# Optimization experiments

Hardware: AMD Instinct MI355X
Metric: run time of the kernel (lower is better)

The kernel has to match this reference:

```python
import jax, jax.numpy as jnp
import numpy as np

N = 30000      # nodes
E = 480000     # edges
H = 128        # hidden_nf
NQ = 7         # qubits
D = 2 ** NQ    # 128, quantum state dim == embedding_size
NL = 2         # block n_layers (QGCL layers)
QL = 2         # quantum circuit layers inside each QGCL
NORM = 100.0   # normalization_factor ('sum' aggregation)
NORM_CONST = 1.0


def _cnot_perm_indices(n):
    # Composed permutation for CNOT(0,1)...CNOT(n-2,n-1), CNOT(n-1,0).
    # PennyLane convention: wire 0 is the most significant bit.
    idx = np.arange(2 ** n)
    pairs = [(i, i + 1) for i in range(n - 1)] + [(n - 1, 0)]
    g = None
    for c, t in pairs:
        cb = (idx >> (n - 1 - c)) & 1
        f = idx ^ (cb << (n - 1 - t))  # flip target bit if control set (involution)
        g = f if g is None else g[f]
    return g

_CNOT_G = jnp.asarray(_cnot_perm_indices(NQ))


def _quantum_states(q_in, coeffs, A_re, A_im):
    """Vectorized VQC over all nodes. q_in [N,D] real -> [N,D] complex state."""
    norm = jnp.sqrt(jnp.sum(q_in ** 2, axis=1, keepdims=True) + 1e-12)
    s = (q_in / norm).astype(jnp.complex64)  # normalized initial state per node
    I = jnp.eye(D, dtype=jnp.complex64)
    for j in range(QL):
        # Cayley transform -> unitary
        A = (A_re[j] + 1j * A_im[j]).astype(jnp.complex64)
        A = A + A.conj().T
        q = (A - 1j * I) @ jnp.linalg.inv(A + 1j * I)
        # single-qubit layer: RY(b) @ RX(a) on every qubit -> kron power
        a, b = coeffs[j, 0].astype(jnp.complex64), coeffs[j, 1].astype(jnp.complex64)
        ca, sa = jnp.cos(a / 2), jnp.sin(a / 2)
        cb, sb = jnp.cos(b / 2), jnp.sin(b / 2)
        RX = jnp.stack([jnp.stack([ca, -1j * sa]), jnp.stack([-1j * sa, ca])])
        RY = jnp.stack([jnp.stack([cb, -sb]), jnp.stack([sb, cb])])
        G = RY @ RX
        Gk = G
        for _ in range(NQ - 1):
            Gk = jnp.kron(Gk, G)
        s = s @ q.T            # QubitUnitary
        s = s @ Gk.T           # RX/RY on all qubits
        s = s[:, _CNOT_G]      # CNOT ring (pure permutation)
    return s


def setup_inputs() -> dict:
    key = jax.random.key(0)
    ks = jax.random.split(key, 20)
    return {
        "h": jax.random.normal(ks[0], (N, H), jnp.float32),
        "x": jax.random.normal(ks[1], (N, 3), jnp.float32),
        "edge_index": jax.random.randint(ks[2], (2, E), 0, N, jnp.int32),
        "edge_attr": jax.random.normal(ks[3], (E, 1), jnp.float32),
        "e_w1": jax.random.normal(ks[4], (NL, 2 * H + 2, H), jnp.float32) * 0.05,
        "e_b1": jnp.zeros((NL, H), jnp.float32),
        "e_w2": jax.random.normal(ks[5], (NL, H, H), jnp.float32) * 0.05,
        "e_b2": jnp.zeros((NL, H), jnp.float32),
        "enc_w": jax.random.normal(ks[6], (NL, 2 * H, D), jnp.float32) * 0.05,
        "enc_b": jnp.zeros((NL, D), jnp.float32),
        "coeffs": jax.random.normal(ks[7], (NL, QL, 2), jnp.float32) * 0.1,
        "A_re": jax.random.normal(ks[8], (NL, QL, D, D), jnp.float32) * 0.01,
        "A_im": jax.random.normal(ks[9], (NL, QL, D, D), jnp.float32) * 0.01,
        "dec_w": jax.random.normal(ks[10], (NL, D, H), jnp.float32) * 0.05,
        "dec_b": jnp.zeros((NL, H), jnp.float32),
        "c_w1": jax.random.normal(ks[11], (2 * H + 2, H), jnp.float32) * 0.05,
        "c_b1": jnp.zeros((H,), jnp.float32),
        "c_w2": jax.random.normal(ks[12], (H, H), jnp.float32) * 0.05,
        "c_b2": jnp.zeros((H,), jnp.float32),
        "c_w3": jax.random.normal(ks[13], (H, 1), jnp.float32) * 0.001,  # xavier gain=0.001
    }


def reference(h, x, edge_index, edge_attr, e_w1, e_b1, e_w2, e_b2, enc_w, enc_b,
              coeffs, A_re, A_im, dec_w, dec_b, c_w1, c_b1, c_w2, c_b2, c_w3):
    row, col = edge_index[0], edge_index[1]
    # coord2diff
    diff = x[row] - x[col]
    radial = jnp.sum(diff ** 2, axis=1, keepdims=True)     # [E,1] (used as 'distances')
    coord_diff = diff / (jnp.sqrt(radial + 1e-8) + NORM_CONST)
    eattr = jnp.concatenate([radial, edge_attr], axis=1)   # [E,2]

    for l in range(NL):  # QGCL layers
        m = jnp.concatenate([h[row], h[col], eattr], axis=1)       # [E, 2H+2]
        m = jax.nn.silu(m @ e_w1[l] + e_b1[l])
        m = jax.nn.silu(m @ e_w2[l] + e_b2[l])                     # edge messages mij
        agg = jax.ops.segment_sum(m, row, num_segments=N) / NORM   # scatter-add
        q_in = jnp.concatenate([h, agg], axis=1) @ enc_w[l] + enc_b[l]
        # quantum part is detached in the original (torch .detach + re-tensor)
        qs = jax.lax.stop_gradient(
            _quantum_states(q_in, coeffs[l], A_re[l], A_im[l]))
        h = h + qs.real.astype(h.dtype) @ dec_w[l] + dec_b[l]

    # EquivariantUpdate (tanh=False)
    t = jnp.concatenate([h[row], h[col], eattr], axis=1)
    t = jax.nn.silu(t @ c_w1 + c_b1)
    t = jax.nn.silu(t @ c_w2 + c_b2)
    t = t @ c_w3                                                   # [E,1]
    trans = coord_diff * t
    x = x + jax.ops.segment_sum(trans, row, num_segments=N) / NORM
    return h, x
```

## Files before the change

### kernel.cpp

```cpp
#include <hip/hip_runtime.h>
#include <math.h>

#define N_NODES 30000
#define N_EDGES 480000
#define HDIM 128
#define EPB 64
#define AS 296
#define NAS 264
#define MS 136

typedef __attribute__((ext_vector_type(8))) short short8b;
typedef __attribute__((ext_vector_type(4))) float f32x4;

__device__ __forceinline__ float silu_f(float v) {
  return v / (1.0f + __expf(-v));
}

__device__ __forceinline__ unsigned short f2bf(float f) {
  unsigned int u = __float_as_uint(f);
  unsigned int r = u + 0x7fffu + ((u >> 16) & 1u);
  return (unsigned short)(r >> 16);
}

__global__ void init_out_kernel(const float* __restrict__ h,
                                const float* __restrict__ x,
                                float* __restrict__ out) {
  int idx = blockIdx.x * 256 + threadIdx.x;
  out[idx] = h[idx];
  if (idx < N_NODES * 3) out[N_NODES * HDIM + idx] = x[idx];
}

__global__ void h_to_bf_kernel(const float* __restrict__ h,
                               ushort* __restrict__ hbf) {
  int idx = blockIdx.x * 256 + threadIdx.x;
  float4 v = ((const float4*)h)[idx];
  ushort4 o;
  o.x = f2bf(v.x); o.y = f2bf(v.y); o.z = f2bf(v.z); o.w = f2bf(v.w);
  ((ushort4*)hbf)[idx] = o;
}

__global__ void convert_w_kernel(const float* __restrict__ W,
                                 ushort* __restrict__ dst, int Kreal, int KT) {
  int idx = blockIdx.x * 256 + threadIdx.x;
  if (idx >= KT * 4096) return;
  int kt = idx >> 12, rem = idx & 4095, n = rem >> 5, kk = rem & 31;
  int k = kt * 32 + kk;
  float v = (k < Kreal) ? W[(size_t)k * HDIM + n] : 0.0f;
  dst[idx] = f2bf(v);
}

__global__ void count_kernel(const int* __restrict__ ei, int* __restrict__ cursor) {
  int e = blockIdx.x * 256 + threadIdx.x;
  atomicAdd(&cursor[ei[e]], 1);
}

__global__ __launch_bounds__(1024) void scan_kernel(int* __restrict__ cursor,
                                                    int* __restrict__ cstart) {
  __shared__ int sums[1024];
  const int tid = threadIdx.x;
  const int base = tid * 30;
  int local[30];
  int s = 0;
#pragma unroll
  for (int j = 0; j < 30; ++j) {
    int idx = base + j;
    int d = (idx < N_NODES) ? cursor[idx] : 0;
    local[j] = s;
    s += d;
  }
  sums[tid] = s;
  __syncthreads();
  for (int off = 1; off < 1024; off <<= 1) {
    int add = (tid >= off) ? sums[tid - off] : 0;
    __syncthreads();
    sums[tid] += add;
    __syncthreads();
  }
  int excl = (tid == 0) ? 0 : sums[tid - 1];
#pragma unroll
  for (int j = 0; j < 30; ++j) {
    int idx = base + j;
    if (idx < N_NODES) {
      int v = excl + local[j];
      cursor[idx] = v;
      cstart[idx] = v;
    }
  }
}

__global__ void fill_kernel(const int* __restrict__ ei, int* __restrict__ cursor,
                            int* __restrict__ elist) {
// ... 115 lines not shown
  gkm[(size_t)lj * 16384 + idx] = acc;
}

__global__ void nj_kernel(const float2* __restrict__ qm,
                          const float2* __restrict__ gkm,
                          const int* __restrict__ g,
                          float2* __restrict__ njm) {
  int lj = blockIdx.y;
  int idx = blockIdx.x * 256 + threadIdx.x;
  int i = idx >> 7, c = idx & 127;
  int gc = g[c];
  const float2* q = qm + (size_t)lj * 16384;
  const float2* gk = gkm + (size_t)lj * 16384;
  float2 acc = make_float2(0.f, 0.f);
  for (int k = 0; k < 128; ++k) {
    float2 qa = q[k * 128 + i];
    float2 gb = gk[gc * 128 + k];
    acc.x += qa.x * gb.x - qa.y * gb.y;
    acc.y += qa.x * gb.y + qa.y * gb.x;
  }
  njm[(size_t)lj * 16384 + idx] = acc;
}

__global__ void compose_kernel(const float2* __restrict__ njm,
                               float2* __restrict__ um) {
  int l = blockIdx.y;
  int idx = blockIdx.x * 256 + threadIdx.x;
  int i = idx >> 7, c = idx & 127;
  const float2* n0 = njm + (size_t)(l * 2 + 0) * 16384;
  const float2* n1 = njm + (size_t)(l * 2 + 1) * 16384;
  float2 acc = make_float2(0.f, 0.f);
  for (int k = 0; k < 128; ++k) {
    float2 a = n0[i * 128 + k];
    float2 b = n1[k * 128 + c];
    acc.x += a.x * b.x - a.y * b.y;
    acc.y += a.x * b.y + a.y * b.x;
  }
  um[(size_t)l * 16384 + idx] = acc;
}

__global__ void wqd_kernel(const float2* __restrict__ um,
                           const float* __restrict__ decw,
                           float* __restrict__ wqd) {
  int l = blockIdx.y;
  int idx = blockIdx.x * 256 + threadIdx.x;
  int i = idx >> 7, c = idx & 127;
  const float2* u = um + (size_t)l * 16384;
  const float* dw = decw + (size_t)l * 16384;
  float acc = 0.f;
  for (int k = 0; k < 128; ++k) acc += u[i * 128 + k].x * dw[k * 128 + c];
  wqd[(size_t)l * 16384 + idx] = acc;
}

__global__ __launch_bounds__(256, 4) void edge_mfma_kernel(
    const ushort* __restrict__ hbf, const int* __restrict__ ei,
    const float* __restrict__ x, const float* __restrict__ ea,
    const int* __restrict__ elist, const int* __restrict__ cstart,
    const ushort* __restrict__ w1cs, const float* __restrict__ b1,
    const ushort* __restrict__ w2cs, const float* __restrict__ b2,
    float* __restrict__ agg, float* __restrict__ headp) {
  __shared__ ushort A[EPB * AS];
  __shared__ int rows[EPB];
  ushort* m1 = A;
  float* m2 = (float*)A;

  const int tid = threadIdx.x;
  const int lane = tid & 63, wave = tid >> 6;
  const int lrow = lane & 15, lq = lane >> 4;
  const int wbase = wave * 32;
  const int woff0 = (wbase + lrow) * 32 + lq * 8;
  const int woff1 = (wbase + 16 + lrow) * 32 + lq * 8;

  const float b1v[2] = {b1[wbase + lrow], b1[wbase + 16 + lrow]};
  const float b2v[2] = {b2[wbase + lrow], b2[wbase + 16 + lrow]};

  const int i0 = blockIdx.x * EPB;
  {
    const int e = tid >> 2, j = tid & 3;
    const int edge = elist[i0 + e];
    const int r = ei[edge], c = ei[N_EDGES + edge];
    if (j == 0) rows[e] = r;
    const uint4* hr = (const uint4*)(hbf + (size_t)r * HDIM + j * 32);
    const uint4* hc = (const uint4*)(hbf + (size_t)c * HDIM + j * 32);
    uint4* d1 = (uint4*)(A + e * AS + j * 32);
    uint4* d2 = (uint4*)(A + e * AS + 128 + j * 32);
    d1[0] = hr[0]; d1[1] = hr[1]; d1[2] = hr[2]; d1[3] = hr[3];
    d2[0] = hc[0]; d2[1] = hc[1]; d2[2] = hc[2]; d2[3] = hc[3];
    if (j == 3) {
      float dx = x[r * 3 + 0] - x[c * 3 + 0];
      float dy = x[r * 3 + 1] - x[c * 3 + 1];
      float dz = x[r * 3 + 2] - x[c * 3 + 2];
      ushort* dst = A + e * AS;
      dst[256] = f2bf(dx * dx + dy * dy + dz * dz);
      dst[257] = f2bf(ea[edge]);
#pragma unroll
      for (int z = 258; z < 288; ++z) dst[z] = 0;
    }
  }
  __syncthreads();

  f32x4 acc[4][2];
#pragma unroll
  for (int mt = 0; mt < 4; ++mt)
#pragma unroll
    for (int nt = 0; nt < 2; ++nt) acc[mt][nt] = (f32x4){0.f, 0.f, 0.f, 0.f};
  {
    short8b wcur0 = *(const short8b*)(w1cs + woff0);
    short8b wcur1 = *(const short8b*)(w1cs + woff1);
#pragma unroll
    for (int kt = 0; kt < 9; ++kt) {
      short8b wn0, wn1;
      if (kt < 8) {
        wn0 = *(const short8b*)(w1cs + (kt + 1) * 4096 + woff0);
        wn1 = *(const short8b*)(w1cs + (kt + 1) * 4096 + woff1);
      }
      short8b af[4];
#pragma unroll
      for (int mt = 0; mt < 4; ++mt)
        af[mt] = *(const short8b*)(A + (mt * 16 + lrow) * AS + kt * 32 + lq * 8);
#pragma unroll
      for (int mt = 0; mt < 4; ++mt) {
        acc[mt][0] = __builtin_amdgcn_mfma_f32_16x16x32_bf16(af[mt], wcur0, acc[mt][0], 0, 0, 0);
        acc[mt][1] = __builtin_amdgcn_mfma_f32_16x16x32_bf16(af[mt], wcur1, acc[mt][1], 0, 0, 0);
      }
      if (kt < 8) { wcur0 = wn0; wcur1 = wn1; }
    }
  }
  __syncthreads();
#pragma unroll
  for (int mt = 0; mt < 4; ++mt)
#pragma unroll
    for (int nt = 0; nt < 2; ++nt)
#pragma unroll
      for (int r = 0; r < 4; ++r)
        m1[(mt * 16 + lq * 4 + r) * MS + wbase + nt * 16 + lrow] =
            f2bf(silu_f(acc[mt][nt][r] + b1v[nt]));
  __syncthreads();

  f32x4 acc2[4][2];
#pragma unroll
  for (int mt = 0; mt < 4; ++mt)
#pragma unroll
    for (int nt = 0; nt < 2; ++nt) acc2[mt][nt] = (f32x4){0.f, 0.f, 0.f, 0.f};
  {
    short8b wcur0 = *(const short8b*)(w2cs + woff0);
    short8b wcur1 = *(const short8b*)(w2cs + woff1);
#pragma unroll
    for (int kt = 0; kt < 4; ++kt) {
      short8b wn0, wn1;
      if (kt < 3) {
        wn0 = *(const short8b*)(w2cs + (kt + 1) * 4096 + woff0);
        wn1 = *(const short8b*)(w2cs + (kt + 1) * 4096 + woff1);
      }
      short8b af[4];
#pragma unroll
      for (int mt = 0; mt < 4; ++mt)
        af[mt] = *(const short8b*)(m1 + (mt * 16 + lrow) * MS + kt * 32 + lq * 8);
#pragma unroll
      for (int mt = 0; mt < 4; ++mt) {
        acc2[mt][0] = __builtin_amdgcn_mfma_f32_16x16x32_bf16(af[mt], wcur0, acc2[mt][0], 0, 0, 0);
        acc2[mt][1] = __builtin_amdgcn_mfma_f32_16x16x32_bf16(af[mt], wcur1, acc2[mt][1], 0, 0, 0);
      }
      if (kt < 3) { wcur0 = wn0; wcur1 = wn1; }
    }
  }
  __syncthreads();
#pragma unroll
  for (int mt = 0; mt < 4; ++mt)
#pragma unroll
    for (int nt = 0; nt < 2; ++nt)
#pragma unroll
      for (int r = 0; r < 4; ++r)
        m2[(mt * 16 + lq * 4 + r) * MS + wbase + nt * 16 + lrow] =
            silu_f(acc2[mt][nt][r] + b2v[nt]);
  __syncthreads();

  const int e2 = tid & 63, cg = tid >> 6, cb = cg * 32;
  const int r_e = rows[e2];
  const bool leader = (e2 == 0) || (rows[e2 - 1] != r_e);
  if (leader) {
    f32x4 sum[8];
#pragma unroll
    for (int q = 0; q < 8; ++q) sum[q] = *(const f32x4*)(m2 + e2 * MS + cb + q * 4);
    int f = e2 + 1;
    while (f < EPB && rows[f] == r_e) {
#pragma unroll
      for (int q = 0; q < 8; ++q) sum[q] += *(const f32x4*)(m2 + f * MS + cb + q * 4);
      ++f;
    }
    float* dst = (e2 == 0 && cstart[r_e] < i0)
                     ? headp + (size_t)blockIdx.x * HDIM + cb
                     : agg + (size_t)r_e * HDIM + cb;
#pragma unroll
    for (int q = 0; q < 8; ++q) *(f32x4*)(dst + q * 4) = sum[q];
  }
}

__global__ __launch_bounds__(256, 2) void node_mfma_kernel(
    float* __restrict__ out_h, const float* __restrict__ agg,
    const int* __restrict__ cstart, const int* __restrict__ cend,
    const float* __restrict__ headp,
    const ushort* __restrict__ enccs, const float* __restrict__ encb,
    const ushort* __restrict__ wqdcs, const float* __restrict__ decb,
    ushort* __restrict__ hbf) {
  __shared__ ushort A[EPB * NAS];
  __shared__ ushort m1[EPB * MS];
  __shared__ float nbuf[4 * EPB];
  const int tid = threadIdx.x;
  const int n0 = blockIdx.x * EPB;

  const int lane = tid & 63, wave = tid >> 6;
  const int lrow = lane & 15, lq = lane >> 4;
  const int wbase = wave * 32;

  short8b wef[8][2], wqf[4][2];
#pragma unroll
  for (int kt = 0; kt < 8; ++kt)
#pragma unroll
    for (int nt = 0; nt < 2; ++nt)
      wef[kt][nt] = *(const short8b*)(enccs + kt * 4096 + (wbase + nt * 16 + lrow) * 32 + lq * 8);
#pragma unroll
  for (int kt = 0; kt < 4; ++kt)
#pragma unroll
    for (int nt = 0; nt < 2; ++nt)
      wqf[kt][nt] = *(const short8b*)(wqdcs + kt * 4096 + (wbase + nt * 16 + lrow) * 32 + lq * 8);
  const float ebv[2] = {encb[wbase + lrow], encb[wbase + 16 + lrow]};
  const float dbv[2] = {decb[wbase + lrow], decb[wbase + 16 + lrow]};

  {
    const int e = tid >> 2, j = tid & 3;
    int node = n0 + e;
    if (node >= N_NODES) node = N_NODES - 1;
    if (j < 2) {
      const float4* s4 = (const float4*)(out_h + (size_t)node * HDIM + j * 64);
      ushort* dst = A + e * NAS + j * 64;
#pragma unroll
      for (int i = 0; i < 16; ++i) {
        float4 v = s4[i];
        ushort4 o;
        o.x = f2bf(v.x); o.y = f2bf(v.y); o.z = f2bf(v.z); o.w = f2bf(v.w);
        ((ushort4*)dst)[i] = o;
      }
    } else {
      const int s = cstart[node], en = cend[node];
      const bool hasAgg = en > s;
      const float4* a4 = (const float4*)(agg + (size_t)node * HDIM + (j - 2) * 64);
      const int bb0 = (s >> 6) + 1;
      const int bb1 = hasAgg ? ((en - 1) >> 6) : 0;
      ushort* dst = A + e * NAS + 128 + (j - 2) * 64;
#pragma unroll
      for (int i = 0; i < 16; ++i) {
        float4 v = hasAgg ? a4[i] : make_float4(0.f, 0.f, 0.f, 0.f);
        for (int bb = bb0; bb <= bb1; ++bb) {
          float4 hv = *(const float4*)(headp + (size_t)bb * HDIM + (j - 2) * 64 + i * 4);
          v.x += hv.x; v.y += hv.y; v.z += hv.z; v.w += hv.w;
        }
        ushort4 o;
        o.x = f2bf(v.x * 0.01f); o.y = f2bf(v.y * 0.01f);
        o.z = f2bf(v.z * 0.01f); o.w = f2bf(v.w * 0.01f);
        ((ushort4*)dst)[i] = o;
      }
    }
  }
  __syncthreads();

  f32x4 acc[4][2];
#pragma unroll
  for (int mt = 0; mt < 4; ++mt)
#pragma unroll
    for (int nt = 0; nt < 2; ++nt) acc[mt][nt] = (f32x4){0.f, 0.f, 0.f, 0.f};
#pragma unroll
  for (int kt = 0; kt < 8; ++kt) {
    short8b af[4];
#pragma unroll
    for (int mt = 0; mt < 4; ++mt)
      af[mt] = *(const short8b*)(A + (mt * 16 + lrow) * NAS + kt * 32 + lq * 8);
#pragma unroll
    for (int mt = 0; mt < 4; ++mt)
#pragma unroll
      for (int nt = 0; nt < 2; ++nt)
        acc[mt][nt] = __builtin_amdgcn_mfma_f32_16x16x32_bf16(af[mt], wef[kt][nt], acc[mt][nt], 0, 0, 0);
  }
#pragma unroll
  for (int mt = 0; mt < 4; ++mt) {
    float ssp[4] = {0.f, 0.f, 0.f, 0.f};
#pragma unroll
    for (int nt = 0; nt < 2; ++nt)
#pragma unroll
      for (int r = 0; r < 4; ++r) {
        acc[mt][nt][r] += ebv[nt];
        ssp[r] += acc[mt][nt][r] * acc[mt][nt][r];
      }
#pragma unroll
    for (int m = 1; m < 16; m <<= 1)
#pragma unroll
      for (int r = 0; r < 4; ++r) ssp[r] += __shfl_xor(ssp[r], m, 64);
    if (lrow == 0) {
#pragma unroll
      for (int r = 0; r < 4; ++r)
        nbuf[wave * EPB + mt * 16 + lq * 4 + r] = ssp[r];
    }
  }
  __syncthreads();
#pragma unroll
  for (int mt = 0; mt < 4; ++mt)
#pragma unroll
    for (int r = 0; r < 4; ++r) {
      const int row = mt * 16 + lq * 4 + r;
      float sum = nbuf[row] + nbuf[EPB + row] + nbuf[2 * EPB + row] + nbuf[3 * EPB + row];
      float inv = 1.0f / sqrtf(sum + 1e-12f);
#pragma unroll
      for (int nt = 0; nt < 2; ++nt)
        m1[row * MS + wbase + nt * 16 + lrow] = f2bf(acc[mt][nt][r] * inv);
    }
  __syncthreads();

  f32x4 acc2[4][2];
#pragma unroll
  for (int mt = 0; mt < 4; ++mt)
#pragma unroll
    for (int nt = 0; nt < 2; ++nt) acc2[mt][nt] = (f32x4){0.f, 0.f, 0.f, 0.f};
#pragma unroll
  for (int kt = 0; kt < 4; ++kt) {
    short8b af[4];
#pragma unroll
    for (int mt = 0; mt < 4; ++mt)
      af[mt] = *(const short8b*)(m1 + (mt * 16 + lrow) * MS + kt * 32 + lq * 8);
#pragma unroll
    for (int mt = 0; mt < 4; ++mt)
#pragma unroll
      for (int nt = 0; nt < 2; ++nt)
        acc2[mt][nt] = __builtin_amdgcn_mfma_f32_16x16x32_bf16(af[mt], wqf[kt][nt], acc2[mt][nt], 0, 0, 0);
  }
#pragma unroll
  for (int mt = 0; mt < 4; ++mt)
#pragma unroll
    for (int nt = 0; nt < 2; ++nt) {
      const int n = wbase + nt * 16 + lrow;
#pragma unroll
      for (int r = 0; r < 4; ++r) {
        const int node = n0 + mt * 16 + lq * 4 + r;
        if (node < N_NODES) {
          size_t off = (size_t)node * HDIM + n;
          float hn = out_h[off] + acc2[mt][nt][r] + dbv[nt];
          out_h[off] = hn;
          hbf[off] = f2bf(hn);
        }
      }
    }
}

__global__ __launch_bounds__(256, 4) void coord_mfma_kernel(
    const ushort* __restrict__ hbf, const int* __restrict__ ei,
    const float* __restrict__ x, const float* __restrict__ ea,
    const int* __restrict__ elist,
    const ushort* __restrict__ w1cs, const float* __restrict__ b1,
    const ushort* __restrict__ w2cs, const float* __restrict__ b2,
    const float* __restrict__ w3, float* __restrict__ xout) {
  __shared__ ushort A[EPB * AS];
  __shared__ int rows[EPB];
  __shared__ int colsA[EPB];
  __shared__ float pbuf[4 * EPB];
  __shared__ float tv[EPB];
  ushort* m1 = A;

  const int tid = threadIdx.x;
  const int lane = tid & 63, wave = tid >> 6;
  const int lrow = lane & 15, lq = lane >> 4;
  const int wbase = wave * 32;
  const int woff0 = (wbase + lrow) * 32 + lq * 8;
  const int woff1 = (wbase + 16 + lrow) * 32 + lq * 8;

  const float b1v[2] = {b1[wbase + lrow], b1[wbase + 16 + lrow]};
  const float b2v[2] = {b2[wbase + lrow], b2[wbase + 16 + lrow]};
  const float w3v[2] = {w3[wbase + lrow], w3[wbase + 16 + lrow]};

  const int i0 = blockIdx.x * EPB;
  {
    const int e = tid >> 2, j = tid & 3;
    const int edge = elist[i0 + e];
    const int r = ei[edge], c = ei[N_EDGES + edge];
    if (j == 0) { rows[e] = r; colsA[e] = c; }
    const uint4* hr = (const uint4*)(hbf + (size_t)r * HDIM + j * 32);
    const uint4* hc = (const uint4*)(hbf + (size_t)c * HDIM + j * 32);
    uint4* d1 = (uint4*)(A + e * AS + j * 32);
    uint4* d2 = (uint4*)(A + e * AS + 128 + j * 32);
    d1[0] = hr[0]; d1[1] = hr[1]; d1[2] = hr[2]; d1[3] = hr[3];
    d2[0] = hc[0]; d2[1] = hc[1]; d2[2] = hc[2]; d2[3] = hc[3];
    if (j == 3) {
      float dx = x[r * 3 + 0] - x[c * 3 + 0];
      float dy = x[r * 3 + 1] - x[c * 3 + 1];
      float dz = x[r * 3 + 2] - x[c * 3 + 2];
      ushort* dst = A + e * AS;
      dst[256] = f2bf(dx * dx + dy * dy + dz * dz);
      dst[257] = f2bf(ea[edge]);
#pragma unroll
      for (int z = 258; z < 288; ++z) dst[z] = 0;
    }
  }
  __syncthreads();

  f32x4 acc[4][2];
#pragma unroll
  for (int mt = 0; mt < 4; ++mt)
#pragma unroll
    for (int nt = 0; nt < 2; ++nt) acc[mt][nt] = (f32x4){0.f, 0.f, 0.f, 0.f};
  {
    short8b wcur0 = *(const short8b*)(w1cs + woff0);
    short8b wcur1 = *(const short8b*)(w1cs + woff1);
#pragma unroll
    for (int kt = 0; kt < 9; ++kt) {
      short8b wn0, wn1;
      if (kt < 8) {
        wn0 = *(const short8b*)(w1cs + (kt + 1) * 4096 + woff0);
        wn1 = *(const short8b*)(w1cs + (kt + 1) * 4096 + woff1);
      }
      short8b af[4];
#pragma unroll
      for (int mt = 0; mt < 4; ++mt)
        af[mt] = *(const short8b*)(A + (mt * 16 + lrow) * AS + kt * 32 + lq * 8);
#pragma unroll
      for (int mt = 0; mt < 4; ++mt) {
        acc[mt][0] = __builtin_amdgcn_mfma_f32_16x16x32_bf16(af[mt], wcur0, acc[mt][0], 0, 0, 0);
        acc[mt][1] = __builtin_amdgcn_mfma_f32_16x16x32_bf16(af[mt], wcur1, acc[mt][1], 0, 0, 0);
      }
      if (kt < 8) { wcur0 = wn0; wcur1 = wn1; }
    }
  }
  __syncthreads();
#pragma unroll
  for (int mt = 0; mt < 4; ++mt)
#pragma unroll
    for (int nt = 0; nt < 2; ++nt)
#pragma unroll
      for (int r = 0; r < 4; ++r)
        m1[(mt * 16 + lq * 4 + r) * MS + wbase + nt * 16 + lrow] =
            f2bf(silu_f(acc[mt][nt][r] + b1v[nt]));
  __syncthreads();

  f32x4 acc2[4][2];
#pragma unroll
  for (int mt = 0; mt < 4; ++mt)
#pragma unroll
    for (int nt = 0; nt < 2; ++nt) acc2[mt][nt] = (f32x4){0.f, 0.f, 0.f, 0.f};
  {
    short8b wcur0 = *(const short8b*)(w2cs + woff0);
    short8b wcur1 = *(const short8b*)(w2cs + woff1);
#pragma unroll
    for (int kt = 0; kt < 4; ++kt) {
      short8b wn0, wn1;
      if (kt < 3) {
        wn0 = *(const short8b*)(w2cs + (kt + 1) * 4096 + woff0);
        wn1 = *(const short8b*)(w2cs + (kt + 1) * 4096 + woff1);
      }
      short8b af[4];
#pragma unroll
      for (int mt = 0; mt < 4; ++mt)
        af[mt] = *(const short8b*)(m1 + (mt * 16 + lrow) * MS + kt * 32 + lq * 8);
#pragma unroll
      for (int mt = 0; mt < 4; ++mt) {
        acc2[mt][0] = __builtin_amdgcn_mfma_f32_16x16x32_bf16(af[mt], wcur0, acc2[mt][0], 0, 0, 0);
        acc2[mt][1] = __builtin_amdgcn_mfma_f32_16x16x32_bf16(af[mt], wcur1, acc2[mt][1], 0, 0, 0);
      }
      if (kt < 3) { wcur0 = wn0; wcur1 = wn1; }
    }
  }
#pragma unroll
  for (int mt = 0; mt < 4; ++mt) {
    float p[4] = {0.f, 0.f, 0.f, 0.f};
#pragma unroll
    for (int nt = 0; nt < 2; ++nt)
#pragma unroll
      for (int r = 0; r < 4; ++r)
        p[r] += silu_f(acc2[mt][nt][r] + b2v[nt]) * w3v[nt];
#pragma unroll
    for (int m = 1; m < 16; m <<= 1)
#pragma unroll
      for (int r = 0; r < 4; ++r) p[r] += __shfl_xor(p[r], m, 64);
    if (lrow == 0) {
#pragma unroll
      for (int r = 0; r < 4; ++r)
        pbuf[wave * EPB + mt * 16 + lq * 4 + r] = p[r];
    }
  }
  __syncthreads();
  if (tid < EPB) {
    tv[tid] = (pbuf[tid] + pbuf[EPB + tid] + pbuf[2 * EPB + tid] + pbuf[3 * EPB + tid]) * 0.01f;
  }
  __syncthreads();
  if (tid < EPB) {
    const int e = tid;
    const int r_e = rows[e];
    const bool leader = (e == 0) || (rows[e - 1] != r_e);
    if (leader) {
      float sx = 0.f, sy = 0.f, sz = 0.f;
      int f = e;
      do {
        const int c = colsA[f];
        float dx = x[r_e * 3 + 0] - x[c * 3 + 0];
        float dy = x[r_e * 3 + 1] - x[c * 3 + 1];
        float dz = x[r_e * 3 + 2] - x[c * 3 + 2];
        float radial = dx * dx + dy * dy + dz * dz;
        float s = 1.0f / (sqrtf(radial + 1e-8f) + 1.0f);
        float t = tv[f];
        sx += dx * s * t; sy += dy * s * t; sz += dz * s * t;
        ++f;
      } while (f < EPB && rows[f] == r_e);
      atomicAdd(&xout[r_e * 3 + 0], sx);
      atomicAdd(&xout[r_e * 3 + 1], sy);
      atomicAdd(&xout[r_e * 3 + 2], sz);
    }
  }
}

extern "C" void kernel_launch(void* const* d_in, const int* in_sizes, int n_in,
                              void* d_out, int out_size, void* d_ws, size_t ws_size,
                              hipStream_t stream) {
  const float* h     = (const float*)d_in[0];
  const float* x     = (const float*)d_in[1];
  const int*   ei    = (const int*)d_in[2];
  const float* ea    = (const float*)d_in[3];
  const float* e_w1  = (const float*)d_in[4];
  const float* e_b1  = (const float*)d_in[5];
  const float* e_w2  = (const float*)d_in[6];
  const float* e_b2  = (const float*)d_in[7];
  const float* enc_w = (const float*)d_in[8];
  const float* enc_b = (const float*)d_in[9];
  const float* coeffs= (const float*)d_in[10];
  const float* A_re  = (const float*)d_in[11];
  const float* A_im  = (const float*)d_in[12];
  const float* dec_w = (const float*)d_in[13];
  const float* dec_b = (const float*)d_in[14];
  const float* c_w1  = (const float*)d_in[15];
  const float* c_b1  = (const float*)d_in[16];
  const float* c_w2  = (const float*)d_in[17];
  const float* c_b2  = (const float*)d_in[18];
  const float* c_w3  = (const float*)d_in[19];

  float* out = (float*)d_out;
  float* ws  = (float*)d_ws;

  float*  agg    = ws;
  float2* xa     = (float2*)(ws + 3840000);
  float2* xb     = (float2*)(ws + 3971072);
  float2* xt     = (float2*)(ws + 4102144);
  float2* qm     = (float2*)(ws + 4233216);
  float2* gkm    = (float2*)(ws + 4364288);
  float2* njm    = (float2*)(ws + 4495360);
  float2* um     = (float2*)(ws + 4626432);
  float*  wqd    = ws + 4691968;
  int*    perm   = (int*)(ws + 4724736);
  int*    cursor = (int*)(ws + 4724864);
  int*    cstart = (int*)(ws + 4754864);
  int*    elist  = (int*)(ws + 4784864);
  float*  headp  = ws + 5264864;
  ushort* hbf    = (ushort*)(ws + 6224864);
  ushort* w1cs   = (ushort*)(ws + 8144864);
  ushort* w2cs   = (ushort*)(ws + 8181728);
  ushort* cw1cs  = (ushort*)(ws + 8198112);
  ushort* cw2cs  = (ushort*)(ws + 8216544);
  ushort* enccs  = (ushort*)(ws + 8224736);
  ushort* wqdcs  = (ushort*)(ws + 8257504);

  init_out_kernel<<<15000, 256, 0, stream>>>(h, x, out);

  hipMemsetAsync(cursor, 0, N_NODES * sizeof(int), stream);
  count_kernel<<<1875, 256, 0, stream>>>(ei, cursor);
  scan_kernel<<<1, 1024, 0, stream>>>(cursor, cstart);
  fill_kernel<<<1875, 256, 0, stream>>>(ei, cursor, elist);

  perm_kernel<<<1, 128, 0, stream>>>(perm);
  ns_init_kernel<<<dim3(64, 4), 256, 0, stream>>>(A_re, A_im, xa);
  float2* cur = xa;
  float2* nxt = xb;
  for (int it = 0; it < 4; ++it) {
    ns_bx_kernel<<<dim3(64, 4), 256, 0, stream>>>(A_re, A_im, cur, xt);
    ns_upd_kernel<<<dim3(64, 4), 256, 0, stream>>>(cur, xt, nxt);
    float2* tmp = cur; cur = nxt; nxt = tmp;
  }
  qmat_kernel<<<dim3(64, 4), 256, 0, stream>>>(A_re, A_im, cur, qm);
  gk_kernel<<<dim3(64, 4), 256, 0, stream>>>(coeffs, gkm);
  nj_kernel<<<dim3(64, 4), 256, 0, stream>>>(qm, gkm, perm, njm);
  compose_kernel<<<dim3(64, 2), 256, 0, stream>>>(njm, um);
  wqd_kernel<<<dim3(64, 2), 256, 0, stream>>>(um, dec_w, wqd);

  for (int l = 0; l < 2; ++l) {
    convert_w_kernel<<<144, 256, 0, stream>>>(e_w1 + (size_t)l * 258 * HDIM,
                                              w1cs + (size_t)l * 9 * 4096, 258, 9);
    convert_w_kernel<<<64, 256, 0, stream>>>(e_w2 + (size_t)l * HDIM * HDIM,
                                             w2cs + (size_t)l * 4 * 4096, 128, 4);
    convert_w_kernel<<<128, 256, 0, stream>>>(enc_w + (size_t)l * 256 * HDIM,
                                              enccs + (size_t)l * 8 * 4096, 256, 8);
    convert_w_kernel<<<64, 256, 0, stream>>>(wqd + (size_t)l * HDIM * HDIM,
                                             wqdcs + (size_t)l * 4 * 4096, 128, 4);
  }
  convert_w_kernel<<<144, 256, 0, stream>>>(c_w1, cw1cs, 258, 9);
  convert_w_kernel<<<64, 256, 0, stream>>>(c_w2, cw2cs, 128, 4);

  h_to_bf_kernel<<<3750, 256, 0, stream>>>(out, hbf);

  for (int l = 0; l < 2; ++l) {
    edge_mfma_kernel<<<N_EDGES / EPB, 256, 0, stream>>>(
        hbf, ei, x, ea, elist, cstart,
        w1cs + (size_t)l * 9 * 4096, e_b1 + l * HDIM,
        w2cs + (size_t)l * 4 * 4096, e_b2 + l * HDIM, agg, headp);
    node_mfma_kernel<<<(N_NODES + EPB - 1) / EPB, 256, 0, stream>>>(
        out, agg, cstart, cursor, headp,
        enccs + (size_t)l * 8 * 4096, enc_b + l * HDIM,
        wqdcs + (size_t)l * 4 * 4096, dec_b + l * HDIM, hbf);
  }

  coord_mfma_kernel<<<N_EDGES / EPB, 256, 0, stream>>>(
      hbf, ei, x, ea, elist, cw1cs, c_b1, cw2cs, c_b2, c_w3,
      out + (size_t)N_NODES * HDIM);
}
```

Baseline: 825.0 us.

## Precompute per-node first-layer projections and store edge aggregates in bf16

The first edge-MLP matmul over [h_row, h_col, eattr] is split algebraically: a new per-node kernel computes h@W1_top and h@W1_bot once per node. Edge kernels then gather these two projections and add the rank-2 edge-attribute terms with scalar FMAs instead of running a K=288 MFMA per edge. This cuts per-edge matmul work by roughly two thirds, though each gathered row is now twice as wide. The aggregation buffers and head partials are also switched from fp32 to bf16 to halve traffic, and the shared buffer is shrunk with raised occupancy bounds, at some precision cost.

```diff
diff --git a/kernel.cpp b/kernel.cpp
--- a/kernel.cpp
+++ b/kernel.cpp
@@ -5,7 +5,6 @@
 #define N_EDGES 480000
 #define HDIM 128
 #define EPB 64
-#define AS 296
 #define NAS 264
 #define MS 136
 
@@ -22,21 +21,16 @@
   return (unsigned short)(r >> 16);
 }
 
+__device__ __forceinline__ float bf2f(unsigned short u) {
+  return __uint_as_float((unsigned int)u << 16);
+}
+
 __global__ void init_out_kernel(const float* __restrict__ h,
                                 const float* __restrict__ x,
                                 float* __restrict__ out) {
   int idx = blockIdx.x * 256 + threadIdx.x;
   out[idx] = h[idx];
   if (idx < N_NODES * 3) out[N_NODES * HDIM + idx] = x[idx];
-}
-
-__global__ void h_to_bf_kernel(const float* __restrict__ h,
-                               ushort* __restrict__ hbf) {
-  int idx = blockIdx.x * 256 + threadIdx.x;
-  float4 v = ((const float4*)h)[idx];
-  ushort4 o;
-  o.x = f2bf(v.x); o.y = f2bf(v.y); o.z = f2bf(v.z); o.w = f2bf(v.w);
-  ((ushort4*)hbf)[idx] = o;
 }
 
 __global__ void convert_w_kernel(const float* __restrict__ W,
@@ -258,17 +252,86 @@
   wqd[(size_t)l * 16384 + idx] = acc;
 }
 
-__global__ __launch_bounds__(256, 4) void edge_mfma_kernel(
-    const ushort* __restrict__ hbf, const int* __restrict__ ei,
+__global__ __launch_bounds__(256, 2) void uv_kernel(
+    const float* __restrict__ h, const ushort* __restrict__ w1cs,
+    ushort* __restrict__ UV) {
+  __shared__ ushort A[EPB * MS];
+  const int tid = threadIdx.x;
+  const int n0 = blockIdx.x * EPB;
+  const int lane = tid & 63, wave = tid >> 6;
+  const int lrow = lane & 15, lq = lane >> 4;
+  const int wbase = wave * 32;
+  const int woff0 = (wbase + lrow) * 32 + lq * 8;
+  const int woff1 = (wbase + 16 + lrow) * 32 + lq * 8;
+
+  {
+    const int e = tid >> 2, j = tid & 3;
+    int node = n0 + e;
+    if (node >= N_NODES) node = N_NODES - 1;
+    const float4* s4 = (const float4*)(h + (size_t)node * HDIM + j * 32);
+    ushort* dst = A + e * MS + j * 32;
+#pragma unroll
+    for (int i = 0; i < 8; ++i) {
+      float4 v = s4[i];
+      ushort4 o;
+      o.x = f2bf(v.x); o.y = f2bf(v.y); o.z = f2bf(v.z); o.w = f2bf(v.w);
+      ((ushort4*)dst)[i] = o;
+    }
+  }
+  __syncthreads();
+
+  f32x4 aU[4][2], aV[4][2];
+#pragma unroll
+  for (int mt = 0; mt < 4; ++mt)
+#pragma unroll
+    for (int nt = 0; nt < 2; ++nt) {
+      aU[mt][nt] = (f32x4){0.f, 0.f, 0.f, 0.f};
+      aV[mt][nt] = (f32x4){0.f, 0.f, 0.f, 0.f};
+    }
+#pragma unroll
+  for (int kt = 0; kt < 4; ++kt) {
+    short8b af[4];
+#pragma unroll
+    for (int mt = 0; mt < 4; ++mt)
+      af[mt] = *(const short8b*)(A + (mt * 16 + lrow) * MS + kt * 32 + lq * 8);
+    short8b u0 = *(const short8b*)(w1cs + kt * 4096 + woff0);
+    short8b u1 = *(const short8b*)(w1cs + kt * 4096 + woff1);
+    short8b v0 = *(const short8b*)(w1cs + (kt + 4) * 4096 + woff0);
+    short8b v1 = *(const short8b*)(w1cs + (kt + 4) * 4096 + woff1);
+#pragma unroll
+    for (int mt = 0; mt < 4; ++mt) {
+      aU[mt][0] = __builtin_amdgcn_mfma_f32_16x16x32_bf16(af[mt], u0, aU[mt][0], 0, 0, 0);
+      aU[mt][1] = __builtin_amdgcn_mfma_f32_16x16x32_bf16(af[mt], u1, aU[mt][1], 0, 0, 0);
+      aV[mt][0] = __builtin_amdgcn_mfma_f32_16x16x32_bf16(af[mt], v0, aV[mt][0], 0, 0, 0);
+      aV[mt][1] = __builtin_amdgcn_mfma_f32_16x16x32_bf16(af[mt], v1, aV[mt][1], 0, 0, 0);
+    }
+  }
+#pragma unroll
+  for (int mt = 0; mt < 4; ++mt)
+#pragma unroll
+    for (int nt = 0; nt < 2; ++nt) {
+      const int col = wbase + nt * 16 + lrow;
+#pragma unroll
+      for (int r = 0; r < 4; ++r) {
+        const int node = n0 + mt * 16 + lq * 4 + r;
+        if (node < N_NODES) {
+          UV[(size_t)node * 256 + col] = f2bf(aU[mt][nt][r]);
+          UV[(size_t)node * 256 + 128 + col] = f2bf(aV[mt][nt][r]);
+        }
+      }
+    }
+}
+
+__global__ __launch_bounds__(256, 8) void edge_mfma_kernel(
+    const ushort* __restrict__ UV, const int* __restrict__ ei,
     const float* __restrict__ x, const float* __restrict__ ea,
     const int* __restrict__ elist, const int* __restrict__ cstart,
     const ushort* __restrict__ w1cs, const float* __restrict__ b1,
     const ushort* __restrict__ w2cs, const float* __restrict__ b2,
-    float* __restrict__ agg, float* __restrict__ headp) {
-  __shared__ ushort A[EPB * AS];
+    ushort* __restrict__ aggb, ushort* __restrict__ headpb) {
+  __shared__ ushort m1[EPB * MS];
+  __shared__ float wrow[384];
   __shared__ int rows[EPB];
-  ushort* m1 = A;
-  float* m2 = (float*)A;
 
   const int tid = threadIdx.x;
   const int lane = tid & 63, wave = tid >> 6;
@@ -276,71 +339,48 @@
   const int wbase = wave * 32;
   const int woff0 = (wbase + lrow) * 32 + lq * 8;
   const int woff1 = (wbase + 16 + lrow) * 32 + lq * 8;
-
-  const float b1v[2] = {b1[wbase + lrow], b1[wbase + 16 + lrow]};
   const float b2v[2] = {b2[wbase + lrow], b2[wbase + 16 + lrow]};
 
+  if (tid < 128) {
+    wrow[tid] = bf2f(w1cs[8 * 4096 + tid * 32 + 0]);
+    wrow[128 + tid] = bf2f(w1cs[8 * 4096 + tid * 32 + 1]);
+    wrow[256 + tid] = b1[tid];
+  }
+
   const int i0 = blockIdx.x * EPB;
-  {
-    const int e = tid >> 2, j = tid & 3;
-    const int edge = elist[i0 + e];
-    const int r = ei[edge], c = ei[N_EDGES + edge];
-    if (j == 0) rows[e] = r;
-    const uint4* hr = (const uint4*)(hbf + (size_t)r * HDIM + j * 32);
-    const uint4* hc = (const uint4*)(hbf + (size_t)c * HDIM + j * 32);
-    uint4* d1 = (uint4*)(A + e * AS + j * 32);
-    uint4* d2 = (uint4*)(A + e * AS + 128 + j * 32);
-    d1[0] = hr[0]; d1[1] = hr[1]; d1[2] = hr[2]; d1[3] = hr[3];
-    d2[0] = hc[0]; d2[1] = hc[1]; d2[2] = hc[2]; d2[3] = hc[3];
-    if (j == 3) {
-      float dx = x[r * 3 + 0] - x[c * 3 + 0];
-      float dy = x[r * 3 + 1] - x[c * 3 + 1];
-      float dz = x[r * 3 + 2] - x[c * 3 + 2];
-      ushort* dst = A + e * AS;
-      dst[256] = f2bf(dx * dx + dy * dy + dz * dz);
-      dst[257] = f2bf(ea[edge]);
-#pragma unroll
-      for (int z = 258; z < 288; ++z) dst[z] = 0;
-    }
-  }
-  __syncthreads();
-
-  f32x4 acc[4][2];
-#pragma unroll
-  for (int mt = 0; mt < 4; ++mt)
-#pragma unroll
-    for (int nt = 0; nt < 2; ++nt) acc[mt][nt] = (f32x4){0.f, 0.f, 0.f, 0.f};
-  {
-    short8b wcur0 = *(const short8b*)(w1cs + woff0);
-    short8b wcur1 = *(const short8b*)(w1cs + woff1);
-#pragma unroll
-    for (int kt = 0; kt < 9; ++kt) {
-      short8b wn0, wn1;
-      if (kt < 8) {
-        wn0 = *(const short8b*)(w1cs + (kt + 1) * 4096 + woff0);
-        wn1 = *(const short8b*)(w1cs + (kt + 1) * 4096 + woff1);
-      }
-      short8b af[4];
-#pragma unroll
-      for (int mt = 0; mt < 4; ++mt)
-        af[mt] = *(const short8b*)(A + (mt * 16 + lrow) * AS + kt * 32 + lq * 8);
-#pragma unroll
-      for (int mt = 0; mt < 4; ++mt) {
-        acc[mt][0] = __builtin_amdgcn_mfma_f32_16x16x32_bf16(af[mt], wcur0, acc[mt][0], 0, 0, 0);
-        acc[mt][1] = __builtin_amdgcn_mfma_f32_16x16x32_bf16(af[mt], wcur1, acc[mt][1], 0, 0, 0);
-      }
-      if (kt < 8) { wcur0 = wn0; wcur1 = wn1; }
-    }
-  }
-  __syncthreads();
-#pragma unroll
-  for (int mt = 0; mt < 4; ++mt)
-#pragma unroll
-    for (int nt = 0; nt < 2; ++nt)
-#pragma unroll
-      for (int r = 0; r < 4; ++r)
-        m1[(mt * 16 + lq * 4 + r) * MS + wbase + nt * 16 + lrow] =
-            f2bf(silu_f(acc[mt][nt][r] + b1v[nt]));
+  const int e = tid >> 2, j = tid & 3;
+  const int edge = elist[i0 + e];
+  const int r = ei[edge], c = ei[N_EDGES + edge];
+  if (j == 0) rows[e] = r;
+  float dx = x[r * 3 + 0] - x[c * 3 + 0];
+  float dy = x[r * 3 + 1] - x[c * 3 + 1];
+  float dz = x[r * 3 + 2] - x[c * 3 + 2];
+  const float radial = dx * dx + dy * dy + dz * dz;
+  const float eav = ea[edge];
+  const uint4* up = (const uint4*)(UV + (size_t)r * 256 + j * 32);
+  const uint4* vp = (const uint4*)(UV + (size_t)c * 256 + 128 + j * 32);
+  uint4 u[4] = {up[0], up[1], up[2], up[3]};
+  uint4 v[4] = {vp[0], vp[1], vp[2], vp[3]};
+  __syncthreads();
+
+#pragma unroll
+  for (int q4 = 0; q4 < 4; ++q4) {
+    const uint* uu = (const uint*)&u[q4];
+    const uint* vv = (const uint*)&v[q4];
+    uint wv[4];
+#pragma unroll
+    for (int t = 0; t < 4; ++t) {
+      const int col = j * 32 + q4 * 8 + t * 2;
+      float a0 = __uint_as_float(uu[t] << 16) + __uint_as_float(vv[t] << 16) + wrow[256 + col];
+      float a1 = __uint_as_float(uu[t] & 0xffff0000u) + __uint_as_float(vv[t] & 0xffff0000u) + wrow[256 + col + 1];
+      a0 = fmaf(radial, wrow[col], a0);
+      a1 = fmaf(radial, wrow[col + 1], a1);
+      a0 = fmaf(eav, wrow[128 + col], a0);
+      a1 = fmaf(eav, wrow[128 + col + 1], a1);
+      wv[t] = (uint)f2bf(silu_f(a0)) | ((uint)f2bf(silu_f(a1)) << 16);
+    }
+    *(uint4*)(m1 + e * MS + j * 32 + q4 * 8) = make_uint4(wv[0], wv[1], wv[2], wv[3]);
+  }
   __syncthreads();
 
   f32x4 acc2[4][2];
@@ -376,39 +416,64 @@
 #pragma unroll
     for (int nt = 0; nt < 2; ++nt)
 #pragma unroll
-      for (int r = 0; r < 4; ++r)
-        m2[(mt * 16 + lq * 4 + r) * MS + wbase + nt * 16 + lrow] =
-            silu_f(acc2[mt][nt][r] + b2v[nt]);
+      for (int r2 = 0; r2 < 4; ++r2)
+        m1[(mt * 16 + lq * 4 + r2) * MS + wbase + nt * 16 + lrow] =
+            f2bf(silu_f(acc2[mt][nt][r2] + b2v[nt]));
   __syncthreads();
 
   const int e2 = tid & 63, cg = tid >> 6, cb = cg * 32;
   const int r_e = rows[e2];
   const bool leader = (e2 == 0) || (rows[e2 - 1] != r_e);
   if (leader) {
-    f32x4 sum[8];
-#pragma unroll
-    for (int q = 0; q < 8; ++q) sum[q] = *(const f32x4*)(m2 + e2 * MS + cb + q * 4);
+    float sum[32];
+    {
+      const uint4* mr = (const uint4*)(m1 + e2 * MS + cb);
+#pragma unroll
+      for (int q4 = 0; q4 < 4; ++q4) {
+        uint4 w = mr[q4];
+        const uint* wp = (const uint*)&w;
+#pragma unroll
+        for (int t = 0; t < 4; ++t) {
+          sum[q4 * 8 + t * 2] = __uint_as_float(wp[t] << 16);
+          sum[q4 * 8 + t * 2 + 1] = __uint_as_float(wp[t] & 0xffff0000u);
+        }
+      }
+    }
     int f = e2 + 1;
     while (f < EPB && rows[f] == r_e) {
-#pragma unroll
-      for (int q = 0; q < 8; ++q) sum[q] += *(const f32x4*)(m2 + f * MS + cb + q * 4);
+      const uint4* mr = (const uint4*)(m1 + f * MS + cb);
+#pragma unroll
+      for (int q4 = 0; q4 < 4; ++q4) {
+        uint4 w = mr[q4];
+        const uint* wp = (const uint*)&w;
+#pragma unroll
+        for (int t = 0; t < 4; ++t) {
+          sum[q4 * 8 + t * 2] += __uint_as_float(wp[t] << 16);
+          sum[q4 * 8 + t * 2 + 1] += __uint_as_float(wp[t] & 0xffff0000u);
+        }
+      }
       ++f;
     }
-    float* dst = (e2 == 0 && cstart[r_e] < i0)
-                     ? headp + (size_t)blockIdx.x * HDIM + cb
-                     : agg + (size_t)r_e * HDIM + cb;
-#pragma unroll
-    for (int q = 0; q < 8; ++q) *(f32x4*)(dst + q * 4) = sum[q];
+    ushort* dstp = (e2 == 0 && cstart[r_e] < i0)
+                       ? headpb + (size_t)blockIdx.x * HDIM + cb
+                       : aggb + (size_t)r_e * HDIM + cb;
+#pragma unroll
+    for (int q4 = 0; q4 < 4; ++q4) {
+      uint wv[4];
+#pragma unroll
+      for (int t = 0; t < 4; ++t)
+        wv[t] = (uint)f2bf(sum[q4 * 8 + t * 2]) | ((uint)f2bf(sum[q4 * 8 + t * 2 + 1]) << 16);
+      *(uint4*)(dstp + q4 * 8) = make_uint4(wv[0], wv[1], wv[2], wv[3]);
+    }
   }
 }
 
 __global__ __launch_bounds__(256, 2) void node_mfma_kernel(
-    float* __restrict__ out_h, const float* __restrict__ agg,
+    float* __restrict__ out_h, const ushort* __restrict__ aggb,
     const int* __restrict__ cstart, const int* __restrict__ cend,
-    const float* __restrict__ headp,
+    const ushort* __restrict__ headpb,
     const ushort* __restrict__ enccs, const float* __restrict__ encb,
-    const ushort* __restrict__ wqdcs, const float* __restrict__ decb,
-    ushort* __restrict__ hbf) {
+    const ushort* __restrict__ wqdcs, const float* __restrict__ decb) {
   __shared__ ushort A[EPB * NAS];
   __shared__ ushort m1[EPB * MS];
   __shared__ float nbuf[4 * EPB];
@@ -450,21 +515,39 @@
     } else {
       const int s = cstart[node], en = cend[node];
       const bool hasAgg = en > s;
-      const float4* a4 = (const float4*)(agg + (size_t)node * HDIM + (j - 2) * 64);
+      const uint4* a4 = (const uint4*)(aggb + (size_t)node * HDIM + (j - 2) * 64);
       const int bb0 = (s >> 6) + 1;
       const int bb1 = hasAgg ? ((en - 1) >> 6) : 0;
       ushort* dst = A + e * NAS + 128 + (j - 2) * 64;
 #pragma unroll
-      for (int i = 0; i < 16; ++i) {
-        float4 v = hasAgg ? a4[i] : make_float4(0.f, 0.f, 0.f, 0.f);
+      for (int i = 0; i < 8; ++i) {
+        float f[8];
+        if (hasAgg) {
+          uint4 w = a4[i];
+          const uint* wp = (const uint*)&w;
+#pragma unroll
+          for (int t = 0; t < 4; ++t) {
+            f[t * 2] = __uint_as_float(wp[t] << 16);
+            f[t * 2 + 1] = __uint_as_float(wp[t] & 0xffff0000u);
+          }
+        } else {
+#pragma unroll
+          for (int t = 0; t < 8; ++t) f[t] = 0.f;
+        }
         for (int bb = bb0; bb <= bb1; ++bb) {
-          float4 hv = *(const float4*)(headp + (size_t)bb * HDIM + (j - 2) * 64 + i * 4);
-          v.x += hv.x; v.y += hv.y; v.z += hv.z; v.w += hv.w;
+          uint4 hw = *(const uint4*)(headpb + (size_t)bb * HDIM + (j - 2) * 64 + i * 8);
+          const uint* hp = (const uint*)&hw;
+#pragma unroll
+          for (int t = 0; t < 4; ++t) {
+            f[t * 2] += __uint_as_float(hp[t] << 16);
+            f[t * 2 + 1] += __uint_as_float(hp[t] & 0xffff0000u);
+          }
         }
-        ushort4 o;
-        o.x = f2bf(v.x * 0.01f); o.y = f2bf(v.y * 0.01f);
-        o.z = f2bf(v.z * 0.01f); o.w = f2bf(v.w * 0.01f);
-        ((ushort4*)dst)[i] = o;
+        uint wv[4];
+#pragma unroll
+        for (int t = 0; t < 4; ++t)
+          wv[t] = (uint)f2bf(f[t * 2] * 0.01f) | ((uint)f2bf(f[t * 2 + 1] * 0.01f) << 16);
+        *(uint4*)(dst + i * 8) = make_uint4(wv[0], wv[1], wv[2], wv[3]);
       }
     }
   }
@@ -548,27 +631,25 @@
         const int node = n0 + mt * 16 + lq * 4 + r;
         if (node < N_NODES) {
           size_t off = (size_t)node * HDIM + n;
-          float hn = out_h[off] + acc2[mt][nt][r] + dbv[nt];
-          out_h[off] = hn;
-          hbf[off] = f2bf(hn);
+          out_h[off] = out_h[off] + acc2[mt][nt][r] + dbv[nt];
         }
       }
     }
 }
 
-__global__ __launch_bounds__(256, 4) void coord_mfma_kernel(
-    const ushort* __restrict__ hbf, const int* __restrict__ ei,
+__global__ __launch_bounds__(256, 7) void coord_mfma_kernel(
+    const ushort* __restrict__ UV, const int* __restrict__ ei,
     const float* __restrict__ x, const float* __restrict__ ea,
     const int* __restrict__ elist,
     const ushort* __restrict__ w1cs, const float* __restrict__ b1,
     const ushort* __restrict__ w2cs, const float* __restrict__ b2,
     const float* __restrict__ w3, float* __restrict__ xout) {
-  __shared__ ushort A[EPB * AS];
+  __shared__ ushort m1[EPB * MS];
+  __shared__ float wrow[384];
   __shared__ int rows[EPB];
   __shared__ int colsA[EPB];
   __shared__ float pbuf[4 * EPB];
   __shared__ float tv[EPB];
-  ushort* m1 = A;
 
   const int tid = threadIdx.x;
   const int lane = tid & 63, wave = tid >> 6;
@@ -576,72 +657,49 @@
   const int wbase = wave * 32;
   const int woff0 = (wbase + lrow) * 32 + lq * 8;
   const int woff1 = (wbase + 16 + lrow) * 32 + lq * 8;
-
-  const float b1v[2] = {b1[wbase + lrow], b1[wbase + 16 + lrow]};
   const float b2v[2] = {b2[wbase + lrow], b2[wbase + 16 + lrow]};
   const float w3v[2] = {w3[wbase + lrow], w3[wbase + 16 + lrow]};
 
+  if (tid < 128) {
+    wrow[tid] = bf2f(w1cs[8 * 4096 + tid * 32 + 0]);
+    wrow[128 + tid] = bf2f(w1cs[8 * 4096 + tid * 32 + 1]);
+    wrow[256 + tid] = b1[tid];
+  }
+
   const int i0 = blockIdx.x * EPB;
-  {
-    const int e = tid >> 2, j = tid & 3;
-    const int edge = elist[i0 + e];
-    const int r = ei[edge], c = ei[N_EDGES + edge];
-    if (j == 0) { rows[e] = r; colsA[e] = c; }
-    const uint4* hr = (const uint4*)(hbf + (size_t)r * HDIM + j * 32);
-    const uint4* hc = (const uint4*)(hbf + (size_t)c * HDIM + j * 32);
-    uint4* d1 = (uint4*)(A + e * AS + j * 32);
-    uint4* d2 = (uint4*)(A + e * AS + 128 + j * 32);
-    d1[0] = hr[0]; d1[1] = hr[1]; d1[2] = hr[2]; d1[3] = hr[3];
-    d2[0] = hc[0]; d2[1] = hc[1]; d2[2] = hc[2]; d2[3] = hc[3];
-    if (j == 3) {
-      float dx = x[r * 3 + 0] - x[c * 3 + 0];
-      float dy = x[r * 3 + 1] - x[c * 3 + 1];
-      float dz = x[r * 3 + 2] - x[c * 3 + 2];
-      ushort* dst = A + e * AS;
-      dst[256] = f2bf(dx * dx + dy * dy + dz * dz);
-      dst[257] = f2bf(ea[edge]);
-#pragma unroll
-      for (int z = 258; z < 288; ++z) dst[z] = 0;
-    }
-  }
-  __syncthreads();
-
-  f32x4 acc[4][2];
-#pragma unroll
-  for (int mt = 0; mt < 4; ++mt)
-#pragma unroll
-    for (int nt = 0; nt < 2; ++nt) acc[mt][nt] = (f32x4){0.f, 0.f, 0.f, 0.f};
-  {
-    short8b wcur0 = *(const short8b*)(w1cs + woff0);
-    short8b wcur1 = *(const short8b*)(w1cs + woff1);
-#pragma unroll
-    for (int kt = 0; kt < 9; ++kt) {
-      short8b wn0, wn1;
-      if (kt < 8) {
-        wn0 = *(const short8b*)(w1cs + (kt + 1) * 4096 + woff0);
-        wn1 = *(const short8b*)(w1cs + (kt + 1) * 4096 + woff1);
-      }
-      short8b af[4];
-#pragma unroll
-      for (int mt = 0; mt < 4; ++mt)
-        af[mt] = *(const short8b*)(A + (mt * 16 + lrow) * AS + kt * 32 + lq * 8);
-#pragma unroll
-      for (int mt = 0; mt < 4; ++mt) {
-        acc[mt][0] = __builtin_amdgcn_mfma_f32_16x16x32_bf16(af[mt], wcur0, acc[mt][0], 0, 0, 0);
-        acc[mt][1] = __builtin_amdgcn_mfma_f32_16x16x32_bf16(af[mt], wcur1, acc[mt][1], 0, 0, 0);
-      }
-      if (kt < 8) { wcur0 = wn0; wcur1 = wn1; }
-    }
-  }
-  __syncthreads();
-#pragma unroll
-  for (int mt = 0; mt < 4; ++mt)
-#pragma unroll
-    for (int nt = 0; nt < 2; ++nt)
-#pragma unroll
-      for (int r = 0; r < 4; ++r)
-        m1[(mt * 16 + lq * 4 + r) * MS + wbase + nt * 16 + lrow] =
-            f2bf(silu_f(acc[mt][nt][r] + b1v[nt]));
+  const int e = tid >> 2, j = tid & 3;
+  const int edge = elist[i0 + e];
+  const int r = ei[edge], c = ei[N_EDGES + edge];
+  if (j == 0) { rows[e] = r; colsA[e] = c; }
+  float dx = x[r * 3 + 0] - x[c * 3 + 0];
+  float dy = x[r * 3 + 1] - x[c * 3 + 1];
+  float dz = x[r * 3 + 2] - x[c * 3 + 2];
+  const float radial = dx * dx + dy * dy + dz * dz;
+  const float eav = ea[edge];
+  const uint4* up = (const uint4*)(UV + (size_t)r * 256 + j * 32);
+  const uint4* vp = (const uint4*)(UV + (size_t)c * 256 + 128 + j * 32);
+  uint4 u[4] = {up[0], up[1], up[2], up[3]};
+  uint4 v[4] = {vp[0], vp[1], vp[2], vp[3]};
+  __syncthreads();
+
+#pragma unroll
+  for (int q4 = 0; q4 < 4; ++q4) {
+    const uint* uu = (const uint*)&u[q4];
+    const uint* vv = (const uint*)&v[q4];
+    uint wv[4];
+#pragma unroll
+    for (int t = 0; t < 4; ++t) {
+      const int col = j * 32 + q4 * 8 + t * 2;
+      float a0 = __uint_as_float(uu[t] << 16) + __uint_as_float(vv[t] << 16) + wrow[256 + col];
+      float a1 = __uint_as_float(uu[t] & 0xffff0000u) + __uint_as_float(vv[t] & 0xffff0000u) + wrow[256 + col + 1];
+      a0 = fmaf(radial, wrow[col], a0);
+      a1 = fmaf(radial, wrow[col + 1], a1);
+      a0 = fmaf(eav, wrow[128 + col], a0);
+      a1 = fmaf(eav, wrow[128 + col + 1], a1);
+      wv[t] = (uint)f2bf(silu_f(a0)) | ((uint)f2bf(silu_f(a1)) << 16);
+    }
+    *(uint4*)(m1 + e * MS + j * 32 + q4 * 8) = make_uint4(wv[0], wv[1], wv[2], wv[3]);
+  }
   __syncthreads();
 
   f32x4 acc2[4][2];
@@ -677,16 +735,16 @@
 #pragma unroll
     for (int nt = 0; nt < 2; ++nt)
 #pragma unroll
-      for (int r = 0; r < 4; ++r)
-        p[r] += silu_f(acc2[mt][nt][r] + b2v[nt]) * w3v[nt];
+      for (int r2 = 0; r2 < 4; ++r2)
+        p[r2] += silu_f(acc2[mt][nt][r2] + b2v[nt]) * w3v[nt];
 #pragma unroll
     for (int m = 1; m < 16; m <<= 1)
 #pragma unroll
-      for (int r = 0; r < 4; ++r) p[r] += __shfl_xor(p[r], m, 64);
+      for (int r2 = 0; r2 < 4; ++r2) p[r2] += __shfl_xor(p[r2], m, 64);
     if (lrow == 0) {
 #pragma unroll
-      for (int r = 0; r < 4; ++r)
-        pbuf[wave * EPB + mt * 16 + lq * 4 + r] = p[r];
+      for (int r2 = 0; r2 < 4; ++r2)
+        pbuf[wave * EPB + mt * 16 + lq * 4 + r2] = p[r2];
     }
   }
   __syncthreads();
@@ -695,21 +753,21 @@
   }
   __syncthreads();
   if (tid < EPB) {
-    const int e = tid;
-    const int r_e = rows[e];
-    const bool leader = (e == 0) || (rows[e - 1] != r_e);
+    const int e3 = tid;
+    const int r_e = rows[e3];
+    const bool leader = (e3 == 0) || (rows[e3 - 1] != r_e);
     if (leader) {
       float sx = 0.f, sy = 0.f, sz = 0.f;
-      int f = e;
+      int f = e3;
       do {
-        const int c = colsA[f];
-        float dx = x[r_e * 3 + 0] - x[c * 3 + 0];
-        float dy = x[r_e * 3 + 1] - x[c * 3 + 1];
-        float dz = x[r_e * 3 + 2] - x[c * 3 + 2];
-        float radial = dx * dx + dy * dy + dz * dz;
-        float s = 1.0f / (sqrtf(radial + 1e-8f) + 1.0f);
+        const int cc = colsA[f];
+        float ddx = x[r_e * 3 + 0] - x[cc * 3 + 0];
+        float ddy = x[r_e * 3 + 1] - x[cc * 3 + 1];
+        float ddz = x[r_e * 3 + 2] - x[cc * 3 + 2];
+        float rad = ddx * ddx + ddy * ddy + ddz * ddz;
+        float s = 1.0f / (sqrtf(rad + 1e-8f) + 1.0f);
         float t = tv[f];
-        sx += dx * s * t; sy += dy * s * t; sz += dz * s * t;
+        sx += ddx * s * t; sy += ddy * s * t; sz += ddz * s * t;
         ++f;
       } while (f < EPB && rows[f] == r_e);
       atomicAdd(&xout[r_e * 3 + 0], sx);
@@ -746,27 +804,27 @@
   float* out = (float*)d_out;
   float* ws  = (float*)d_ws;
 
-  float*  agg    = ws;
-  float2* xa     = (float2*)(ws + 3840000);
-  float2* xb     = (float2*)(ws + 3971072);
-  float2* xt     = (float2*)(ws + 4102144);
-  float2* qm     = (float2*)(ws + 4233216);
-  float2* gkm    = (float2*)(ws + 4364288);
-  float2* njm    = (float2*)(ws + 4495360);
-  float2* um     = (float2*)(ws + 4626432);
-  float*  wqd    = ws + 4691968;
-  int*    perm   = (int*)(ws + 4724736);
-  int*    cursor = (int*)(ws + 4724864);
-  int*    cstart = (int*)(ws + 4754864);
-  int*    elist  = (int*)(ws + 4784864);
-  float*  headp  = ws + 5264864;
-  ushort* hbf    = (ushort*)(ws + 6224864);
-  ushort* w1cs   = (ushort*)(ws + 8144864);
-  ushort* w2cs   = (ushort*)(ws + 8181728);
-  ushort* cw1cs  = (ushort*)(ws + 8198112);
-  ushort* cw2cs  = (ushort*)(ws + 8216544);
-  ushort* enccs  = (ushort*)(ws + 8224736);
-  ushort* wqdcs  = (ushort*)(ws + 8257504);
+  ushort* aggb   = (ushort*)ws;
+  int*    cursor = (int*)(ws + 1920000);
+  int*    cstart = (int*)(ws + 1950000);
+  int*    elist  = (int*)(ws + 1980000);
+  ushort* headpb = (ushort*)(ws + 2460000);
+  ushort* w1cs   = (ushort*)(ws + 2940000);
+  ushort* w2cs   = (ushort*)(ws + 2976864);
+  ushort* cw1cs  = (ushort*)(ws + 2993248);
+  ushort* cw2cs  = (ushort*)(ws + 3011680);
+  ushort* enccs  = (ushort*)(ws + 3019872);
+  ushort* wqdcs  = (ushort*)(ws + 3052640);
+  int*    perm   = (int*)(ws + 3069024);
+  ushort* UVb    = (ushort*)(ws + 3069152);
+  float2* xa  = (float2*)(ws + 3069152);
+  float2* xb  = (float2*)(ws + 3069152 + 131072);
+  float2* xt  = (float2*)(ws + 3069152 + 262144);
+  float2* qm  = (float2*)(ws + 3069152 + 393216);
+  float2* gkm = (float2*)(ws + 3069152 + 524288);
+  float2* njm = (float2*)(ws + 3069152 + 655360);
+  float2* um  = (float2*)(ws + 3069152 + 786432);
+  float*  wqd = ws + 3069152 + 851968;
 
   init_out_kernel<<<15000, 256, 0, stream>>>(h, x, out);
 
@@ -803,20 +861,21 @@
   convert_w_kernel<<<144, 256, 0, stream>>>(c_w1, cw1cs, 258, 9);
   convert_w_kernel<<<64, 256, 0, stream>>>(c_w2, cw2cs, 128, 4);
 
-  h_to_bf_kernel<<<3750, 256, 0, stream>>>(out, hbf);
-
+  const int NB = (N_NODES + EPB - 1) / EPB;
   for (int l = 0; l < 2; ++l) {
+    uv_kernel<<<NB, 256, 0, stream>>>(out, w1cs + (size_t)l * 9 * 4096, UVb);
     edge_mfma_kernel<<<N_EDGES / EPB, 256, 0, stream>>>(
-        hbf, ei, x, ea, elist, cstart,
+        UVb, ei, x, ea, elist, cstart,
         w1cs + (size_t)l * 9 * 4096, e_b1 + l * HDIM,
-        w2cs + (size_t)l * 4 * 4096, e_b2 + l * HDIM, agg, headp);
-    node_mfma_kernel<<<(N_NODES + EPB - 1) / EPB, 256, 0, stream>>>(
-        out, agg, cstart, cursor, headp,
+        w2cs + (size_t)l * 4 * 4096, e_b2 + l * HDIM, aggb, headpb);
+    node_mfma_kernel<<<NB, 256, 0, stream>>>(
+        out, aggb, cstart, cursor, headpb,
         enccs + (size_t)l * 8 * 4096, enc_b + l * HDIM,
-        wqdcs + (size_t)l * 4 * 4096, dec_b + l * HDIM, hbf);
-  }
-
+        wqdcs + (size_t)l * 4 * 4096, dec_b + l * HDIM);
+  }
+
+  uv_kernel<<<NB, 256, 0, stream>>>(out, cw1cs, UVb);
   coord_mfma_kernel<<<N_EDGES / EPB, 256, 0, stream>>>(
-      hbf, ei, x, ea, elist, cw1cs, c_b1, cw2cs, c_b2, c_w3,
+      UVb, ei, x, ea, elist, cw1cs, c_b1, cw2cs, c_b2, c_w3,
       out + (size_t)N_NODES * HDIM);
 }
```

Result: slower. 885.9 us (+7.4%).
